# Performance work log

Hardware: AMD Instinct MI355X
Metric: run time of the kernel (lower is better)

## Reference

```python
import jax, jax.numpy as jnp
import numpy as np

N = 8192        # nodes
IN_DIM = 512    # input feature dim
H = 8           # heads (hardcoded as 8 in original forward)
HID = 64        # out_feats per head
T = 10          # top-K threshold from settings['T']
OUT = 3         # classes
NEG = -9e15
NE_HALF = 131072  # half edges; graph made symmetric -> 262144 edges


def setup_inputs() -> dict:
    key = jax.random.key(0)
    ks = jax.random.split(key, 10)
    feat = jax.random.normal(ks[0], (N, IN_DIM), jnp.float32)

    def edges(k):
        k1, k2, k3 = jax.random.split(k, 3)
        u = jax.random.randint(k1, (NE_HALF,), 0, N, jnp.int32)
        v = jax.random.randint(k2, (NE_HALF,), 0, N, jnp.int32)
        src = jnp.concatenate([u, v])
        dst = jnp.concatenate([v, u])
        t = jax.random.uniform(k3, (NE_HALF,), jnp.float32) * 0.1  # TransM values
        trans = jnp.concatenate([t, t])
        return src, dst, trans

    src0, dst0, trans0 = edges(ks[1])
    src1, dst1, trans1 = edges(ks[2])
    fc_w0 = jax.random.normal(ks[3], (IN_DIM, H * HID), jnp.float32) * 0.05
    fc_w1 = jax.random.normal(ks[4], (IN_DIM, H * HID), jnp.float32) * 0.05
    sem_w1 = jax.random.normal(ks[5], (H * HID, 128), jnp.float32) * 0.05
    sem_b1 = jnp.zeros((128,), jnp.float32)
    sem_w2 = jax.random.normal(ks[6], (128,), jnp.float32) * 0.05
    lin_w = jax.random.normal(ks[7], (H * HID, OUT), jnp.float32) * 0.05
    lin_b = jnp.zeros((OUT,), jnp.float32)
    return dict(feat=feat, src0=src0, dst0=dst0, trans0=trans0,
                src1=src1, dst1=dst1, trans1=trans1,
                fc_w0=fc_w0, fc_w1=fc_w1, sem_w1=sem_w1, sem_b1=sem_b1,
                sem_w2=sem_w2, lin_w=lin_w, lin_b=lin_b)


def _rohe_conv(feat, src, dst, trans, fc_w):
    f = (feat @ fc_w).reshape(N, H, HID)               # (N,H,HID) projected feats
    # per-edge per-head dot products (same math as dense matmul + edge gather)
    e = jnp.einsum('ehd,ehd->eh', f[src], f[dst])      # (Ne,H)
    vals = trans * e.sum(-1)                           # (Ne,)  (e * e_trans).sum over heads
    # dense sparse->to_dense attn matrix, duplicates coalesced by sum
    A = jnp.zeros((N, N), f.dtype).at[src, dst].add(vals)
    kth = jax.lax.top_k(A, T)[0][:, -1]                # per-row T-th largest
    thr = jnp.maximum(kth, 0.0)                        # clamp(min=0)
    Am = jnp.where(A < thr[:, None], NEG, A)
    gathered = Am[dst, src]                            # == Am.T[src, dst]
    e = jnp.where((gathered < -100.0)[:, None], NEG, e)
    # edge softmax grouped by destination node, per head
    m = jax.ops.segment_max(e, dst, num_segments=N)
    ex = jnp.exp(e - m[dst])
    s = jax.ops.segment_sum(ex, dst, num_segments=N)
    a = ex / s[dst]                                    # (Ne,H)
    # u_mul_e + sum aggregation
    out = jax.ops.segment_sum(f[src] * a[:, :, None], dst, num_segments=N)
    return jax.nn.elu(out).reshape(N, H * HID)         # activation=F.elu, flatten(1)


def reference(feat, src0, dst0, trans0, src1, dst1, trans1,
              fc_w0, fc_w1, sem_w1, sem_b1, sem_w2, lin_w, lin_b):
    z0 = _rohe_conv(feat, src0, dst0, trans0, fc_w0)
    z1 = _rohe_conv(feat, src1, dst1, trans1, fc_w1)
    z = jnp.stack([z0, z1], axis=1)                    # (N, M=2, D)
    # SemanticAttention: project -> tanh -> score, mean over nodes, softmax over metapaths
    w = jnp.tanh(z @ sem_w1 + sem_b1) @ sem_w2         # (N, M)
    beta = jax.nn.softmax(w.mean(0))                   # (M,)
    h = (z * beta[None, :, None]).sum(1)               # (N, D)
    return h @ lin_w + lin_b                           # final nn.Linear
```

## Files before the change

### kernel.cpp

```cpp
#include <hip/hip_runtime.h>
#include <math.h>

#define NN      8192
#define DIM     512
#define NHEAD   8
#define HID     64
#define NE      262144
#define NE_HALF 131072
#define CMASK   (NE_HALF - 1)
#define TOPK    10
#define NEGV    -9e15f
#define MAXD    160

typedef __attribute__((ext_vector_type(8))) short short8;
typedef __attribute__((ext_vector_type(4))) float f32x4;
typedef __attribute__((ext_vector_type(2))) int i32x2;
typedef __attribute__((ext_vector_type(4))) int i32x4;

__device__ __forceinline__ float bf2f(unsigned int h) {
    return __uint_as_float(h << 16);
}
__device__ __forceinline__ unsigned short f2bf(float x) {
    unsigned int u = __float_as_uint(x);
    unsigned int r = (u + 0x7fff + ((u >> 16) & 1)) >> 16;
    return (unsigned short)r;
}

__device__ __forceinline__ void scatter_body(int j, int c,
                                             const int* __restrict__ src0,
                                             const int* __restrict__ src1,
                                             const int* __restrict__ dst0,
                                             const int* __restrict__ dst1,
                                             const float* __restrict__ trans0,
                                             const float* __restrict__ trans1,
                                             int* curF, int* curC,
                                             i32x2* __restrict__ ed,
                                             i32x4* __restrict__ ce) {
    const int* s = c ? src1 : src0;
    const int* dt = c ? dst1 : dst0;
    int v = s[j];
    int dv = dt[j];
    int p = atomicAdd(&curF[c * NN + v], 1);
    i32x2 pk; pk.x = j; pk.y = dv;
    ed[c * NE + p] = pk;
    if (j < NE_HALF) {
        const float* tr = c ? trans1 : trans0;
        int q = atomicAdd(&curC[c * NN + v], 1);
        i32x4 ck;
        ck.x = j; ck.y = dv; ck.z = __float_as_int(tr[j]); ck.w = 0;
        ce[c * NE_HALF + q] = ck;
    }
}

__device__ __forceinline__ void split_w_body(const float* __restrict__ W,
                                             unsigned short* __restrict__ Th,
                                             unsigned short* __restrict__ Tl,
                                             int n0, int k0, int ncols,
                                             float (*t)[33], int tid) {
    int tx = tid & 31, ty = tid >> 5;
    #pragma unroll
    for (int i = 0; i < 4; i++)
        t[ty + 8 * i][tx] = W[(size_t)(k0 + ty + 8 * i) * ncols + n0 + tx];
    __syncthreads();
    #pragma unroll
    for (int i = 0; i < 4; i++) {
        float x = t[tx][ty + 8 * i];
        unsigned short h = f2bf(x);
        size_t off = (size_t)(n0 + ty + 8 * i) * DIM + k0 + tx;
        Th[off] = h;
        Tl[off] = f2bf(x - bf2f(h));
    }
}

__global__ __launch_bounds__(256) void prep(const float* __restrict__ feat,
                                            const float* __restrict__ w1,
                                            const float* __restrict__ fcw0,
                                            const float* __restrict__ fcw1,
                                            unsigned short* __restrict__ fH,
                                            unsigned short* __restrict__ fL,
                                            unsigned short* __restrict__ W1hT,
                                            unsigned short* __restrict__ W1lT,
                                            unsigned short* __restrict__ BhT0,
                                            unsigned short* __restrict__ BlT0,
                                            unsigned short* __restrict__ BhT1,
                                            unsigned short* __restrict__ BlT1,
                                            const int* __restrict__ src0,
                                            const int* __restrict__ src1,
                                            int* __restrict__ countsF,
                                            int* __restrict__ countsC) {
    int b = blockIdx.x;
    __shared__ float t[32][33];
    if (b < 4096) {
        int i = b * 256 + threadIdx.x;
        float4 v = ((const float4*)feat)[i];
        unsigned short h0 = f2bf(v.x), h1 = f2bf(v.y), h2 = f2bf(v.z), h3 = f2bf(v.w);
        ushort4 hv; hv.x = h0; hv.y = h1; hv.z = h2; hv.w = h3;
        ushort4 lv;
        lv.x = f2bf(v.x - bf2f(h0));
        lv.y = f2bf(v.y - bf2f(h1));
        lv.z = f2bf(v.z - bf2f(h2));
        lv.w = f2bf(v.w - bf2f(h3));
        ((ushort4*)fH)[i] = hv;
        ((ushort4*)fL)[i] = lv;
    } else if (b < 4160) {
        int idx = b - 4096;
        split_w_body(w1, W1hT, W1lT, (idx & 3) * 32, (idx >> 2) * 32, 128, t, threadIdx.x);
    } else if (b < 4416) {
        int idx = b - 4160;
        split_w_body(fcw0, BhT0, BlT0, (idx & 15) * 32, (idx >> 4) * 32, DIM, t, threadIdx.x);
    } else if (b < 4672) {
        int idx = b - 4416;
        split_w_body(fcw1, BhT1, BlT1, (idx & 15) * 32, (idx >> 4) * 32, DIM, t, threadIdx.x);
    } else {
        int sb = b - 4672;
        int c = sb >> 10;
        int j = (sb & 1023) * 256 + threadIdx.x;
        const int* s = c ? src1 : src0;
        int v = s[j];
        atomicAdd(&countsF[c * NN + v], 1);
        if (j < NE_HALF) atomicAdd(&countsC[c * NN + v], 1);
    }
}

__global__ __launch_bounds__(256) void gemm_mfma_sc(const unsigned short* __restrict__ Ah,
                                                    const unsigned short* __restrict__ Al,
                                                    const unsigned short* __restrict__ Bh,
                                                    const unsigned short* __restrict__ Bl,
                                                    float* __restrict__ Cf,
                                                    unsigned short* __restrict__ Ch,
                                                    const int* __restrict__ src0,
                                                    const int* __restrict__ src1,
                                                    const int* __restrict__ dst0,
                                                    const int* __restrict__ dst1,
                                                    const float* __restrict__ trans0,
                                                    const float* __restrict__ trans1,
                                                    int* curF, int* curC,
                                                    i32x2* __restrict__ ed,
                                                    i32x4* __restrict__ ce) {
    __shared__ unsigned short Ash[128][32];
    __shared__ unsigned short Asl[128][32];
    __shared__ unsigned short Bsh[64][32];
    __shared__ unsigned short Bsl[64][32];
    const int b = blockIdx.x;
    const int tid = threadIdx.x;
    if (b >= 512) {
        int sb = b - 512;
        int c = sb >> 10;
        int j = (sb & 1023) * 256 + tid;
        scatter_body(j, c, src0, src1, dst0, dst1, trans0, trans1,
                     curF, curC, ed, ce);
        return;
    }
    const int bm = (b >> 3) * 128;
    const int bn = (b & 7) * 64;
    const int lane = tid & 63;
    const int wave = tid >> 6;
    const int wm = (wave >> 1) * 64, wn = (wave & 1) * 32;
    const int fr = lane & 15, fq = lane >> 4;
    const int sr = tid >> 2, sc = (tid & 3) * 8;
    f32x4 acc[4][2] = {};
    const unsigned short* Ahg = Ah + (size_t)(bm + sr) * DIM + sc;
    const unsigned short* Alg = Al + (size_t)(bm + sr) * DIM + sc;
    const unsigned short* Bhg = Bh + (size_t)(bn + sr) * DIM + sc;
    const unsigned short* Blg = Bl + (size_t)(bn + sr) * DIM + sc;
    for (int kb = 0; kb < DIM; kb += 32) {
        __syncthreads();
        __builtin_amdgcn_global_load_lds(
            (const __attribute__((address_space(1))) void*)(Ahg + kb),
            (__attribute__((address_space(3))) void*)(&Ash[sr][sc]), 16, 0, 0);
        __builtin_amdgcn_global_load_lds(
            (const __attribute__((address_space(1))) void*)(Ahg + (size_t)64 * DIM + kb),
            (__attribute__((address_space(3))) void*)(&Ash[sr + 64][sc]), 16, 0, 0);
        __builtin_amdgcn_global_load_lds(
            (const __attribute__((address_space(1))) void*)(Alg + kb),
            (__attribute__((address_space(3))) void*)(&Asl[sr][sc]), 16, 0, 0);
        __builtin_amdgcn_global_load_lds(
            (const __attribute__((address_space(1))) void*)(Alg + (size_t)64 * DIM + kb),
            (__attribute__((address_space(3))) void*)(&Asl[sr + 64][sc]), 16, 0, 0);
        if (sr < 64) {
            __builtin_amdgcn_global_load_lds(
                (const __attribute__((address_space(1))) void*)(Bhg + kb),
                (__attribute__((address_space(3))) void*)(&Bsh[sr][sc]), 16, 0, 0);
            __builtin_amdgcn_global_load_lds(
                (const __attribute__((address_space(1))) void*)(Blg + kb),
                (__attribute__((address_space(3))) void*)(&Bsl[sr][sc]), 16, 0, 0);
        }
        __syncthreads();
        short8 ah[4], al[4], bh[2], bl[2];
        #pragma unroll
        for (int i = 0; i < 4; i++) {
            ah[i] = *(const short8*)&Ash[wm + i * 16 + fr][fq * 8];
            al[i] = *(const short8*)&Asl[wm + i * 16 + fr][fq * 8];
        }
        #pragma unroll
        for (int i = 0; i < 2; i++) {
            bh[i] = *(const short8*)&Bsh[wn + i * 16 + fr][fq * 8];
            bl[i] = *(const short8*)&Bsl[wn + i * 16 + fr][fq * 8];
        }
        #pragma unroll
        for (int mi = 0; mi < 4; mi++)
            #pragma unroll
            for (int ni = 0; ni < 2; ni++) {
                acc[mi][ni] = __builtin_amdgcn_mfma_f32_16x16x32_bf16(ah[mi], bh[ni], acc[mi][ni], 0, 0, 0);
                acc[mi][ni] = __builtin_amdgcn_mfma_f32_16x16x32_bf16(al[mi], bh[ni], acc[mi][ni], 0, 0, 0);
                acc[mi][ni] = __builtin_amdgcn_mfma_f32_16x16x32_bf16(ah[mi], bl[ni], acc[mi][ni], 0, 0, 0);
            }
    }
    #pragma unroll
    for (int mi = 0; mi < 4; mi++)
        #pragma unroll
        for (int ni = 0; ni < 2; ni++)
            #pragma unroll
            for (int r = 0; r < 4; r++) {
                int row = bm + wm + mi * 16 + fq * 4 + r;
                int col = bn + wn + ni * 16 + fr;
                float v = acc[mi][ni][r];
                size_t off = (size_t)row * DIM + col;
                Cf[off] = v;
                Ch[off] = f2bf(v);
            }
}

__global__ __launch_bounds__(256) void scan_offs4(const int* __restrict__ counts,
                                                  int* __restrict__ offs,
                                                  int* __restrict__ cur) {
    int b = blockIdx.x;
    counts += b * NN; offs += b * (NN + 1); cur += b * NN;
    __shared__ int part[256];
    int t = threadIdx.x;
    int base = t * 32;
    int s = 0;
    for (int i = 0; i < 32; i++) s += counts[base + i];
    part[t] = s;
    __syncthreads();
    if (t == 0) {
        int run = 0;
        for (int i = 0; i < 256; i++) { int v = part[i]; part[i] = run; run += v; }
        offs[NN] = run;
    }
    __syncthreads();
    int run = part[t];
    for (int i = 0; i < 32; i++) {
        offs[base + i] = run;
        cur[base + i] = run;
        run += counts[base + i];
    }
}

__global__ __launch_bounds__(256) void edge_dots_csr(const float* __restrict__ Cf,
                                                     const int* __restrict__ coffs,
                                                     const i32x4* __restrict__ ce,
                                                     float* __restrict__ e,
                                                     float* __restrict__ vals) {
    int n = blockIdx.x;
    int s0 = coffs[n];
    int d = coffs[n + 1] - s0;
    if (d <= 0) return;
    int wave = threadIdx.x >> 6, lane = threadIdx.x & 63;
    const float4* pf = (const float4*)(Cf + (size_t)n * DIM);
    float4 f0 = pf[lane * 2], f1 = pf[lane * 2 + 1];
    for (int i = wave; i < d; i += 8) {
        i32x4 c0e = ce[s0 + i];
        int j0 = c0e.x, dj0 = c0e.y;
        float t0 = __int_as_float(c0e.z);
        int i1 = i + 4;
        bool has1 = i1 < d;
        i32x4 c1e = has1 ? ce[s0 + i1] : c0e;
        int j1 = c1e.x, dj1 = c1e.y;
        float t1 = has1 ? __int_as_float(c1e.z) : 0.f;
        const float4* q0 = (const float4*)(Cf + (size_t)dj0 * DIM);
        const float4* q1 = (const float4*)(Cf + (size_t)dj1 * DIM);
        float4 b00 = q0[lane * 2], b01 = q0[lane * 2 + 1];
        float4 b10 = q1[lane * 2], b11 = q1[lane * 2 + 1];
        float p0, p1;
        p0  = f0.x * b00.x + f0.y * b00.y + f0.z * b00.z + f0.w * b00.w;
        p0 += f1.x * b01.x + f1.y * b01.y + f1.z * b01.z + f1.w * b01.w;
        p1  = f0.x * b10.x + f0.y * b10.y + f0.z * b10.z + f0.w * b10.w;
        p1 += f1.x * b11.x + f1.y * b11.y + f1.z * b11.z + f1.w * b11.w;
        p0 += __shfl_xor(p0, 1);
        p0 += __shfl_xor(p0, 2);
        p0 += __shfl_xor(p0, 4);
        p1 += __shfl_xor(p1, 1);
        p1 += __shfl_xor(p1, 2);
        p1 += __shfl_xor(p1, 4);
        if ((lane & 7) == 0) e[(size_t)j0 * NHEAD + (lane >> 3)] = p0;
        if (has1 && (lane & 7) == 0) e[(size_t)j1 * NHEAD + (lane >> 3)] = p1;
        p0 += __shfl_xor(p0, 8);
        p0 += __shfl_xor(p0, 16);
        p0 += __shfl_xor(p0, 32);
        p1 += __shfl_xor(p1, 8);
        p1 += __shfl_xor(p1, 16);
        p1 += __shfl_xor(p1, 32);
        if (lane == 0) {
            vals[j0] = t0 * p0;
            if (has1) vals[j1] = t1 * p1;
        }
    }
}

__global__ __launch_bounds__(256) void conv_post(const int* __restrict__ offs,
                                                 const i32x2* __restrict__ ed,
                                                 const float* __restrict__ e,
                                                 const float* __restrict__ vals,
                                                 const unsigned short* __restrict__ fb,
                                                 unsigned short* __restrict__ zb) {
    const int tid = threadIdx.x;
    const int w = tid >> 6, lane = tid & 63;
    const int n = blockIdx.x * 4 + w;
    int s0 = offs[n];
    int d = offs[n + 1] - s0;
    if (d > MAXD) d = MAXD;
    __shared__ int   ssrc[4][MAXD];
    __shared__ int   sjc[4][MAXD];
    __shared__ float sval[4][MAXD];
    __shared__ float svc[4][MAXD];
    __shared__ unsigned char lead[4][MAXD];
    __shared__ short sk[4][MAXD];
    __shared__ float sms[4][2][NHEAD];
    __shared__ int nkept[4];

    for (int i = lane; i < d; i += 64) {
        i32x2 pk = ed[s0 + i];
        int jc = pk.x & CMASK;
        sjc[w][i] = jc;
        ssrc[w][i] = pk.y;
        sval[w][i] = vals[jc];
    }
    __syncthreads();
    for (int i = lane; i < d; i += 64) {
        int c = ssrc[w][i];
        float sum = 0.f;
        bool leader = true;
        for (int k = 0; k < d; k++) {
            if (ssrc[w][k] == c) {
                sum += sval[w][k];
                if (k < i) leader = false;
            }
        }
        svc[w][i] = sum;
        lead[w][i] = leader ? 1 : 0;
    }
    __syncthreads();
    {
        float v[3];
        #pragma unroll
        for (int s = 0; s < 3; s++) v[s] = -1.f;
        int cnt = 0;
        #pragma unroll
        for (int s = 0; s < 3; s++) {
            int i = lane + s * 64;
            if (i < d && lead[w][i] && svc[w][i] > 0.f) { v[s] = svc[w][i]; cnt++; }
        }
        cnt += __shfl_xor(cnt, 1);  cnt += __shfl_xor(cnt, 2);
        cnt += __shfl_xor(cnt, 4);  cnt += __shfl_xor(cnt, 8);
        cnt += __shfl_xor(cnt, 16); cnt += __shfl_xor(cnt, 32);
        float thr = 0.f;
        if (cnt >= TOPK) {
            unsigned long long key = 0;
            for (int t = 0; t < TOPK; t++) {
                unsigned int bb = 0; int bs = 0;
                #pragma unroll
                for (int s = 0; s < 3; s++) {
                    if (v[s] > 0.f) {
                        unsigned int b = __float_as_uint(v[s]);
                        if (b > bb) { bb = b; bs = s; }
                    }
                }
                key = ((unsigned long long)bb << 12) | (unsigned)(lane << 3) | (unsigned)bs;
                unsigned long long o;
                o = __shfl_xor(key, 1);  if (o > key) key = o;
                o = __shfl_xor(key, 2);  if (o > key) key = o;
                o = __shfl_xor(key, 4);  if (o > key) key = o;
                o = __shfl_xor(key, 8);  if (o > key) key = o;
                o = __shfl_xor(key, 16); if (o > key) key = o;
                o = __shfl_xor(key, 32); if (o > key) key = o;
                int owner = (int)((key >> 3) & 63);
                if (owner == lane) v[key & 7] = -1.f;
            }
            thr = __uint_as_float((unsigned int)(key >> 12));
        }
        int base = 0;
        for (int s = 0; s * 64 < d; s++) {
            int i = s * 64 + lane;
            bool kp = (i < d) && (svc[w][i] >= thr);
            unsigned long long m = __ballot(kp);
            int pos = base + __popcll(m & ((1ull << lane) - 1ull));
            if (kp) sk[w][pos] = (short)i;
            base += (int)__popcll(m);
        }
        if (base == 0) {
            for (int i = lane; i < d; i += 64) sk[w][i] = (short)i;
            if (lane == 0) nkept[w] = -d;
        } else if (lane == 0) nkept[w] = base;
    }
    __syncthreads();
    int nk = nkept[w];
    bool uni = nk < 0;
    int dk = uni ? -nk : nk;
    if (!uni) {
        int h = lane & 7, sub = lane >> 3;
        float m = -INFINITY;
        for (int k = sub; k < dk; k += 8)
            m = fmaxf(m, e[(size_t)sjc[w][sk[w][k]] * NHEAD + h]);
        m = fmaxf(m, __shfl_xor(m, 8));
        m = fmaxf(m, __shfl_xor(m, 16));
        m = fmaxf(m, __shfl_xor(m, 32));
        float s = 0.f;
        for (int k = sub; k < dk; k += 8)
            s += expf(e[(size_t)sjc[w][sk[w][k]] * NHEAD + h] - m);
        s += __shfl_xor(s, 8);
        s += __shfl_xor(s, 16);
        s += __shfl_xor(s, 32);
        if (sub == 0) { sms[w][0][h] = m; sms[w][1][h] = s; }
    }
    __syncthreads();
    int c0 = lane * 8;
    int h = lane >> 3;
    float m = sms[w][0][h], s = sms[w][1][h];
    float invd = 1.0f / (float)d;
    float a0 = 0.f, a1 = 0.f, a2 = 0.f, a3 = 0.f;
    float a4 = 0.f, a5 = 0.f, a6 = 0.f, a7 = 0.f;
    for (int k = 0; k < dk; k++) {
        int ii = sk[w][k];
        float wgt = uni ? invd
                        : expf(e[(size_t)sjc[w][ii] * NHEAD + h] - m) / s;
        uint4 v = *(const uint4*)(fb + (size_t)ssrc[w][ii] * DIM + c0);
        a0 += wgt * bf2f(v.x & 0xffffu); a1 += wgt * bf2f(v.x >> 16);
        a2 += wgt * bf2f(v.y & 0xffffu); a3 += wgt * bf2f(v.y >> 16);
        a4 += wgt * bf2f(v.z & 0xffffu); a5 += wgt * bf2f(v.z >> 16);
        a6 += wgt * bf2f(v.w & 0xffffu); a7 += wgt * bf2f(v.w >> 16);
    }
    a0 = a0 > 0.f ? a0 : expf(a0) - 1.f;
    a1 = a1 > 0.f ? a1 : expf(a1) - 1.f;
    a2 = a2 > 0.f ? a2 : expf(a2) - 1.f;
    a3 = a3 > 0.f ? a3 : expf(a3) - 1.f;
    a4 = a4 > 0.f ? a4 : expf(a4) - 1.f;
    a5 = a5 > 0.f ? a5 : expf(a5) - 1.f;
    a6 = a6 > 0.f ? a6 : expf(a6) - 1.f;
    a7 = a7 > 0.f ? a7 : expf(a7) - 1.f;
    uint4 o;
    o.x = (unsigned)f2bf(a0) | ((unsigned)f2bf(a1) << 16);
    o.y = (unsigned)f2bf(a2) | ((unsigned)f2bf(a3) << 16);
    o.z = (unsigned)f2bf(a4) | ((unsigned)f2bf(a5) << 16);
    o.w = (unsigned)f2bf(a6) | ((unsigned)f2bf(a7) << 16);
    *(uint4*)(zb + (size_t)n * DIM + c0) = o;
}

__global__ __launch_bounds__(256) void sem_scores3(const unsigned short* __restrict__ z0,
                                                   const unsigned short* __restrict__ z1,
                                                   const unsigned short* __restrict__ W1hT,
                                                   const unsigned short* __restrict__ W1lT,
                                                   const float* __restrict__ b1,
                                                   const float* __restrict__ w2,
                                                   float* wsum) {
    const unsigned short* Z = blockIdx.y ? z1 : z0;
    const int bm = blockIdx.x * 64;
    const int tid = threadIdx.x;
    const int lane = tid & 63, wave = tid >> 6;
    const int fr = lane & 15, fq = lane >> 4;
    __shared__ unsigned short Zs[64][32];
    __shared__ unsigned short Wh[128][32];
    __shared__ unsigned short Wl[128][32];
    const int sr = tid >> 2, sc = (tid & 3) * 8;
    f32x4 acc[8] = {};
    const unsigned short* Zg  = Z    + (size_t)(bm + sr) * DIM + sc;
    const unsigned short* Whg = W1hT + (size_t)sr * DIM + sc;
    const unsigned short* Wlg = W1lT + (size_t)sr * DIM + sc;
    for (int kb = 0; kb < DIM; kb += 32) {
        __syncthreads();
        __builtin_amdgcn_global_load_lds(
            (const __attribute__((address_space(1))) void*)(Zg + kb),
            (__attribute__((address_space(3))) void*)(&Zs[sr][sc]), 16, 0, 0);
        __builtin_amdgcn_global_load_lds(
            (const __attribute__((address_space(1))) void*)(Whg + kb),
            (__attribute__((address_space(3))) void*)(&Wh[sr][sc]), 16, 0, 0);
        __builtin_amdgcn_global_load_lds(
            (const __attribute__((address_space(1))) void*)(Whg + (size_t)64 * DIM + kb),
            (__attribute__((address_space(3))) void*)(&Wh[sr + 64][sc]), 16, 0, 0);
        __builtin_amdgcn_global_load_lds(
            (const __attribute__((address_space(1))) void*)(Wlg + kb),
            (__attribute__((address_space(3))) void*)(&Wl[sr][sc]), 16, 0, 0);
        __builtin_amdgcn_global_load_lds(
            (const __attribute__((address_space(1))) void*)(Wlg + (size_t)64 * DIM + kb),
            (__attribute__((address_space(3))) void*)(&Wl[sr + 64][sc]), 16, 0, 0);
        __syncthreads();
        short8 af = *(const short8*)&Zs[wave * 16 + fr][fq * 8];
        #pragma unroll
        for (int ni = 0; ni < 8; ni++) {
            short8 bh = *(const short8*)&Wh[ni * 16 + fr][fq * 8];
            acc[ni] = __builtin_amdgcn_mfma_f32_16x16x32_bf16(af, bh, acc[ni], 0, 0, 0);
        }
        #pragma unroll
        for (int ni = 0; ni < 8; ni++) {
            short8 bl = *(const short8*)&Wl[ni * 16 + fr][fq * 8];
            acc[ni] = __builtin_amdgcn_mfma_f32_16x16x32_bf16(af, bl, acc[ni], 0, 0, 0);
        }
    }
    float local = 0.f;
    #pragma unroll
    for (int ni = 0; ni < 8; ni++) {
        int col = ni * 16 + fr;
        float bb = b1[col], ww = w2[col];
        #pragma unroll
        for (int r = 0; r < 4; r++)
            local += tanhf(acc[ni][r] + bb) * ww;
    }
    __shared__ float red[256];
    red[tid] = local;
    __syncthreads();
    for (int s = 128; s > 0; s >>= 1) {
        if (tid < s) red[tid] += red[tid + s];
        __syncthreads();
    }
    if (tid == 0) atomicAdd(&wsum[blockIdx.y], red[0]);
}

__global__ __launch_bounds__(256) void final_out(const unsigned short* __restrict__ z0,
                                                 const unsigned short* __restrict__ z1,
                                                 const float* __restrict__ wsum,
                                                 const float* __restrict__ lin_w,
                                                 const float* __restrict__ lin_b,
                                                 float* __restrict__ out) {
    int idx = blockIdx.x * 256 + threadIdx.x;
    int n = idx / 3, o = idx - n * 3;
    float w0 = wsum[0] * (1.0f / NN), w1v = wsum[1] * (1.0f / NN);
    float mx = fmaxf(w0, w1v);
    float e0 = expf(w0 - mx), e1 = expf(w1v - mx);
    float beta0 = e0 / (e0 + e1), beta1 = e1 / (e0 + e1);
    const unsigned short* p0 = z0 + (size_t)n * DIM;
    const unsigned short* p1 = z1 + (size_t)n * DIM;
    float acc = 0.f;
    for (int dd = 0; dd < DIM; dd++)
        acc += (beta0 * bf2f(p0[dd]) + beta1 * bf2f(p1[dd])) * lin_w[dd * 3 + o];
    out[idx] = acc + lin_b[o];
}

extern "C" void kernel_launch(void* const* d_in, const int* in_sizes, int n_in,
                              void* d_out, int out_size, void* d_ws, size_t ws_size,
                              hipStream_t stream) {
    const float* feat = (const float*)d_in[0];
    const int*   srcp[2]   = { (const int*)d_in[1], (const int*)d_in[4] };
    const int*   dstp[2]   = { (const int*)d_in[2], (const int*)d_in[5] };
    const float* transp[2] = { (const float*)d_in[3], (const float*)d_in[6] };
    const float* fcw[2]    = { (const float*)d_in[7], (const float*)d_in[8] };
    const float* sem_w1 = (const float*)d_in[9];
    const float* sem_b1 = (const float*)d_in[10];
    const float* sem_w2 = (const float*)d_in[11];
    const float* lin_w  = (const float*)d_in[12];
    const float* lin_b  = (const float*)d_in[13];
    float* out = (float*)d_out;

    char* ws = (char*)d_ws;
    const size_t MB = 1 << 20;
    const size_t KB = 1 << 10;
    if (ws_size < 76 * MB) return;
    float*          Cf    = (float*)(ws);
    unsigned short* Ch    = (unsigned short*)(ws + 16 * MB);
    unsigned short* z0    = (unsigned short*)(ws + 24 * MB);
    unsigned short* z1    = (unsigned short*)(ws + 32 * MB);
    unsigned short* fH    = (unsigned short*)(ws + 40 * MB);
    unsigned short* fL    = (unsigned short*)(ws + 48 * MB);
    float*          e     = (float*)(ws + 56 * MB);
    float*          vals  = (float*)(ws + 60 * MB);
    i32x2*          ed    = (i32x2*)(ws + 60 * MB + 512 * KB);
    i32x4*          ce    = (i32x4*)(ws + 64 * MB + 512 * KB);
    unsigned short* BhT0  = (unsigned short*)(ws + 68 * MB + 512 * KB);
    unsigned short* BlT0  = (unsigned short*)(ws + 69 * MB);
    unsigned short* BhT1  = (unsigned short*)(ws + 69 * MB + 512 * KB);
    unsigned short* BlT1  = (unsigned short*)(ws + 70 * MB);
    unsigned short* W1hT  = (unsigned short*)(ws + 70 * MB + 512 * KB);
    unsigned short* W1lT  = (unsigned short*)(ws + 70 * MB + 640 * KB);
    int*            counts= (int*)  (ws + 70 * MB + 768 * KB);
    int*            offs  = (int*)  (ws + 70 * MB + 896 * KB);
    int*            cur   = (int*)  (ws + 71 * MB + 128 * KB);
    float*          wsum  = (float*)(ws + 71 * MB + 256 * KB);

    hipMemsetAsync(counts, 0, 4 * NN * sizeof(int), stream);
    prep<<<6720, 256, 0, stream>>>(feat, sem_w1, fcw[0], fcw[1],
                                   fH, fL, W1hT, W1lT, BhT0, BlT0, BhT1, BlT1,
                                   srcp[0], srcp[1], counts, counts + 2 * NN);
    scan_offs4<<<4, 256, 0, stream>>>(counts, offs, cur);
    for (int c = 0; c < 2; c++) {
        unsigned short* z = c ? z1 : z0;
        const int* offsF = offs + c * (NN + 1);
        const int* offsC = offs + (2 + c) * (NN + 1);
        const unsigned short* Bh = c ? BhT1 : BhT0;
        const unsigned short* Bl = c ? BlT1 : BlT0;
        int nblk = (c == 0) ? 2560 : 512;
        gemm_mfma_sc<<<nblk, 256, 0, stream>>>(fH, fL, Bh, Bl, Cf, Ch,
                                               srcp[0], srcp[1], dstp[0], dstp[1],
                                               transp[0], transp[1],
                                               cur, cur + 2 * NN, ed, ce);
        edge_dots_csr<<<NN, 256, 0, stream>>>(Cf, offsC, ce + c * NE_HALF, e, vals);
        conv_post<<<NN / 4, 256, 0, stream>>>(offsF, ed + c * NE, e, vals, Ch, z);
    }
    hipMemsetAsync(wsum, 0, 2 * sizeof(float), stream);
    sem_scores3<<<dim3(NN / 64, 2), 256, 0, stream>>>(z0, z1, W1hT, W1lT, sem_b1, sem_w2, wsum);
    final_out<<<(NN * 3) / 256, 256, 0, stream>>>(z0, z1, wsum, lin_w, lin_b, out);
}
```

Measured before the change: 386.1 us.

## Fuse metapath stages across kernels with double-buffered intermediates to overlap work

Splits the per-metapath intermediate buffers (projected features, edge scores, vals) into separate copies for each metapath so the stages of the two metapaths can run in the same launches. The GEMM for metapath 1 now shares a launch with metapath 0's edge dots, and metapath 0's conv shares a launch with metapath 1's edge dots, so there are fewer sequential launches and less tail idle time. The cost is a larger workspace and heterogeneous blocks within a launch, with possible LDS-driven occupancy limits when the GEMM and edge bodies share a kernel.

```diff
diff --git a/kernel.cpp b/kernel.cpp
--- a/kernel.cpp
+++ b/kernel.cpp
@@ -50,6 +50,288 @@
         ck.x = j; ck.y = dv; ck.z = __float_as_int(tr[j]); ck.w = 0;
         ce[c * NE_HALF + q] = ck;
     }
+}
+
+__device__ __forceinline__ void gemm_body(int b,
+                                          const unsigned short* __restrict__ Ah,
+                                          const unsigned short* __restrict__ Al,
+                                          const unsigned short* __restrict__ Bh,
+                                          const unsigned short* __restrict__ Bl,
+                                          float* __restrict__ Cf,
+                                          unsigned short* __restrict__ Ch) {
+    __shared__ unsigned short Ash[128][32];
+    __shared__ unsigned short Asl[128][32];
+    __shared__ unsigned short Bsh[64][32];
+    __shared__ unsigned short Bsl[64][32];
+    const int bm = (b >> 3) * 128;
+    const int bn = (b & 7) * 64;
+    const int tid = threadIdx.x;
+    const int lane = tid & 63;
+    const int wave = tid >> 6;
+    const int wm = (wave >> 1) * 64, wn = (wave & 1) * 32;
+    const int fr = lane & 15, fq = lane >> 4;
+    const int sr = tid >> 2, sc = (tid & 3) * 8;
+    f32x4 acc[4][2] = {};
+    const unsigned short* Ahg = Ah + (size_t)(bm + sr) * DIM + sc;
+    const unsigned short* Alg = Al + (size_t)(bm + sr) * DIM + sc;
+    const unsigned short* Bhg = Bh + (size_t)(bn + sr) * DIM + sc;
+    const unsigned short* Blg = Bl + (size_t)(bn + sr) * DIM + sc;
+    for (int kb = 0; kb < DIM; kb += 32) {
+        __syncthreads();
+        __builtin_amdgcn_global_load_lds(
+            (const __attribute__((address_space(1))) void*)(Ahg + kb),
+            (__attribute__((address_space(3))) void*)(&Ash[sr][sc]), 16, 0, 0);
+        __builtin_amdgcn_global_load_lds(
+            (const __attribute__((address_space(1))) void*)(Ahg + (size_t)64 * DIM + kb),
+            (__attribute__((address_space(3))) void*)(&Ash[sr + 64][sc]), 16, 0, 0);
+        __builtin_amdgcn_global_load_lds(
+            (const __attribute__((address_space(1))) void*)(Alg + kb),
+            (__attribute__((address_space(3))) void*)(&Asl[sr][sc]), 16, 0, 0);
+        __builtin_amdgcn_global_load_lds(
+            (const __attribute__((address_space(1))) void*)(Alg + (size_t)64 * DIM + kb),
+            (__attribute__((address_space(3))) void*)(&Asl[sr + 64][sc]), 16, 0, 0);
+        if (sr < 64) {
+            __builtin_amdgcn_global_load_lds(
+                (const __attribute__((address_space(1))) void*)(Bhg + kb),
+                (__attribute__((address_space(3))) void*)(&Bsh[sr][sc]), 16, 0, 0);
+            __builtin_amdgcn_global_load_lds(
+                (const __attribute__((address_space(1))) void*)(Blg + kb),
+                (__attribute__((address_space(3))) void*)(&Bsl[sr][sc]), 16, 0, 0);
+        }
+        __syncthreads();
+        short8 ah[4], al[4], bh[2], bl[2];
+        #pragma unroll
+        for (int i = 0; i < 4; i++) {
+            ah[i] = *(const short8*)&Ash[wm + i * 16 + fr][fq * 8];
+            al[i] = *(const short8*)&Asl[wm + i * 16 + fr][fq * 8];
+        }
+        #pragma unroll
+        for (int i = 0; i < 2; i++) {
+            bh[i] = *(const short8*)&Bsh[wn + i * 16 + fr][fq * 8];
+            bl[i] = *(const short8*)&Bsl[wn + i * 16 + fr][fq * 8];
+        }
+        #pragma unroll
+        for (int mi = 0; mi < 4; mi++)
+            #pragma unroll
+            for (int ni = 0; ni < 2; ni++) {
+                acc[mi][ni] = __builtin_amdgcn_mfma_f32_16x16x32_bf16(ah[mi], bh[ni], acc[mi][ni], 0, 0, 0);
+                acc[mi][ni] = __builtin_amdgcn_mfma_f32_16x16x32_bf16(al[mi], bh[ni], acc[mi][ni], 0, 0, 0);
+                acc[mi][ni] = __builtin_amdgcn_mfma_f32_16x16x32_bf16(ah[mi], bl[ni], acc[mi][ni], 0, 0, 0);
+            }
+    }
+    #pragma unroll
+    for (int mi = 0; mi < 4; mi++)
+        #pragma unroll
+        for (int ni = 0; ni < 2; ni++)
+            #pragma unroll
+            for (int r = 0; r < 4; r++) {
+                int row = bm + wm + mi * 16 + fq * 4 + r;
+                int col = bn + wn + ni * 16 + fr;
+                float v = acc[mi][ni][r];
+                size_t off = (size_t)row * DIM + col;
+                Cf[off] = v;
+                Ch[off] = f2bf(v);
+            }
+}
+
+__device__ __forceinline__ void edge_body(int n,
+                                          const float* __restrict__ Cf,
+                                          const int* __restrict__ coffs,
+                                          const i32x4* __restrict__ ce,
+                                          float* __restrict__ e,
+                                          float* __restrict__ vals) {
+    int s0 = coffs[n];
+    int d = coffs[n + 1] - s0;
+    if (d <= 0) return;
+    int wave = threadIdx.x >> 6, lane = threadIdx.x & 63;
+    const float4* pf = (const float4*)(Cf + (size_t)n * DIM);
+    float4 f0 = pf[lane * 2], f1 = pf[lane * 2 + 1];
+    for (int i = wave; i < d; i += 8) {
+        i32x4 c0e = ce[s0 + i];
+        int j0 = c0e.x, dj0 = c0e.y;
+        float t0 = __int_as_float(c0e.z);
+        int i1 = i + 4;
+        bool has1 = i1 < d;
+        i32x4 c1e = has1 ? ce[s0 + i1] : c0e;
+        int j1 = c1e.x, dj1 = c1e.y;
+        float t1 = has1 ? __int_as_float(c1e.z) : 0.f;
+        const float4* q0 = (const float4*)(Cf + (size_t)dj0 * DIM);
+        const float4* q1 = (const float4*)(Cf + (size_t)dj1 * DIM);
+        float4 b00 = q0[lane * 2], b01 = q0[lane * 2 + 1];
+        float4 b10 = q1[lane * 2], b11 = q1[lane * 2 + 1];
+        float p0, p1;
+        p0  = f0.x * b00.x + f0.y * b00.y + f0.z * b00.z + f0.w * b00.w;
+        p0 += f1.x * b01.x + f1.y * b01.y + f1.z * b01.z + f1.w * b01.w;
+        p1  = f0.x * b10.x + f0.y * b10.y + f0.z * b10.z + f0.w * b10.w;
+        p1 += f1.x * b11.x + f1.y * b11.y + f1.z * b11.z + f1.w * b11.w;
+        p0 += __shfl_xor(p0, 1);
+        p0 += __shfl_xor(p0, 2);
+        p0 += __shfl_xor(p0, 4);
+        p1 += __shfl_xor(p1, 1);
+        p1 += __shfl_xor(p1, 2);
+        p1 += __shfl_xor(p1, 4);
+        if ((lane & 7) == 0) e[(size_t)j0 * NHEAD + (lane >> 3)] = p0;
+        if (has1 && (lane & 7) == 0) e[(size_t)j1 * NHEAD + (lane >> 3)] = p1;
+        p0 += __shfl_xor(p0, 8);
+        p0 += __shfl_xor(p0, 16);
+        p0 += __shfl_xor(p0, 32);
+        p1 += __shfl_xor(p1, 8);
+        p1 += __shfl_xor(p1, 16);
+        p1 += __shfl_xor(p1, 32);
+        if (lane == 0) {
+            vals[j0] = t0 * p0;
+            if (has1) vals[j1] = t1 * p1;
+        }
+    }
+}
+
+__device__ __forceinline__ void conv_body(int blk,
+                                          const int* __restrict__ offs,
+                                          const i32x2* __restrict__ ed,
+                                          const float* __restrict__ e,
+                                          const float* __restrict__ vals,
+                                          const unsigned short* __restrict__ fb,
+                                          unsigned short* __restrict__ zb) {
+    const int tid = threadIdx.x;
+    const int w = tid >> 6, lane = tid & 63;
+    const int n = blk * 4 + w;
+    int s0 = offs[n];
+    int d = offs[n + 1] - s0;
+    if (d > MAXD) d = MAXD;
+    __shared__ int   ssrc[4][MAXD];
+    __shared__ int   sjc[4][MAXD];
+    __shared__ float sval[4][MAXD];
+    __shared__ float svc[4][MAXD];
+    __shared__ unsigned char lead[4][MAXD];
+    __shared__ short sk[4][MAXD];
+    __shared__ float sms[4][2][NHEAD];
+    __shared__ int nkept[4];
+
+    for (int i = lane; i < d; i += 64) {
+        i32x2 pk = ed[s0 + i];
+        int jc = pk.x & CMASK;
+        sjc[w][i] = jc;
+        ssrc[w][i] = pk.y;
+        sval[w][i] = vals[jc];
+    }
+    __syncthreads();
+    for (int i = lane; i < d; i += 64) {
+        int c = ssrc[w][i];
+        float sum = 0.f;
+        bool leader = true;
+        for (int k = 0; k < d; k++) {
+            if (ssrc[w][k] == c) {
+                sum += sval[w][k];
+                if (k < i) leader = false;
+            }
+        }
+        svc[w][i] = sum;
+        lead[w][i] = leader ? 1 : 0;
+    }
+    __syncthreads();
+    {
+        float v[3];
+        #pragma unroll
+        for (int s = 0; s < 3; s++) v[s] = -1.f;
+        int cnt = 0;
+        #pragma unroll
+        for (int s = 0; s < 3; s++) {
+            int i = lane + s * 64;
+            if (i < d && lead[w][i] && svc[w][i] > 0.f) { v[s] = svc[w][i]; cnt++; }
+        }
+        cnt += __shfl_xor(cnt, 1);  cnt += __shfl_xor(cnt, 2);
+        cnt += __shfl_xor(cnt, 4);  cnt += __shfl_xor(cnt, 8);
+        cnt += __shfl_xor(cnt, 16); cnt += __shfl_xor(cnt, 32);
+        float thr = 0.f;
+        if (cnt >= TOPK) {
+            unsigned long long key = 0;
+            for (int t = 0; t < TOPK; t++) {
+                unsigned int bb = 0; int bs = 0;
+                #pragma unroll
+                for (int s = 0; s < 3; s++) {
+                    if (v[s] > 0.f) {
+                        unsigned int b = __float_as_uint(v[s]);
+                        if (b > bb) { bb = b; bs = s; }
+                    }
+                }
+                key = ((unsigned long long)bb << 12) | (unsigned)(lane << 3) | (unsigned)bs;
+                unsigned long long o;
+                o = __shfl_xor(key, 1);  if (o > key) key = o;
+                o = __shfl_xor(key, 2);  if (o > key) key = o;
+                o = __shfl_xor(key, 4);  if (o > key) key = o;
+                o = __shfl_xor(key, 8);  if (o > key) key = o;
+                o = __shfl_xor(key, 16); if (o > key) key = o;
+                o = __shfl_xor(key, 32); if (o > key) key = o;
+                int owner = (int)((key >> 3) & 63);
+                if (owner == lane) v[key & 7] = -1.f;
+            }
+            thr = __uint_as_float((unsigned int)(key >> 12));
+        }
+        int base = 0;
+        for (int s = 0; s * 64 < d; s++) {
+            int i = s * 64 + lane;
+            bool kp = (i < d) && (svc[w][i] >= thr);
+            unsigned long long m = __ballot(kp);
+            int pos = base + __popcll(m & ((1ull << lane) - 1ull));
+            if (kp) sk[w][pos] = (short)i;
+            base += (int)__popcll(m);
+        }
+        if (base == 0) {
+            for (int i = lane; i < d; i += 64) sk[w][i] = (short)i;
+            if (lane == 0) nkept[w] = -d;
+        } else if (lane == 0) nkept[w] = base;
+    }
+    __syncthreads();
+    int nk = nkept[w];
+    bool uni = nk < 0;
+    int dk = uni ? -nk : nk;
+    if (!uni) {
+        int h = lane & 7, sub = lane >> 3;
+        float m = -INFINITY;
+        for (int k = sub; k < dk; k += 8)
+            m = fmaxf(m, e[(size_t)sjc[w][sk[w][k]] * NHEAD + h]);
+        m = fmaxf(m, __shfl_xor(m, 8));
+        m = fmaxf(m, __shfl_xor(m, 16));
+        m = fmaxf(m, __shfl_xor(m, 32));
+        float s = 0.f;
+        for (int k = sub; k < dk; k += 8)
+            s += expf(e[(size_t)sjc[w][sk[w][k]] * NHEAD + h] - m);
+        s += __shfl_xor(s, 8);
+        s += __shfl_xor(s, 16);
+        s += __shfl_xor(s, 32);
+        if (sub == 0) { sms[w][0][h] = m; sms[w][1][h] = s; }
+    }
+    __syncthreads();
+    int c0 = lane * 8;
+    int h = lane >> 3;
+    float m = sms[w][0][h], s = sms[w][1][h];
+    float invd = 1.0f / (float)d;
+    float a0 = 0.f, a1 = 0.f, a2 = 0.f, a3 = 0.f;
+    float a4 = 0.f, a5 = 0.f, a6 = 0.f, a7 = 0.f;
+    for (int k = 0; k < dk; k++) {
+        int ii = sk[w][k];
+        float wgt = uni ? invd
+                        : expf(e[(size_t)sjc[w][ii] * NHEAD + h] - m) / s;
+        uint4 v = *(const uint4*)(fb + (size_t)ssrc[w][ii] * DIM + c0);
+        a0 += wgt * bf2f(v.x & 0xffffu); a1 += wgt * bf2f(v.x >> 16);
+        a2 += wgt * bf2f(v.y & 0xffffu); a3 += wgt * bf2f(v.y >> 16);
+        a4 += wgt * bf2f(v.z & 0xffffu); a5 += wgt * bf2f(v.z >> 16);
+        a6 += wgt * bf2f(v.w & 0xffffu); a7 += wgt * bf2f(v.w >> 16);
+    }
+    a0 = a0 > 0.f ? a0 : expf(a0) - 1.f;
+    a1 = a1 > 0.f ? a1 : expf(a1) - 1.f;
+    a2 = a2 > 0.f ? a2 : expf(a2) - 1.f;
+    a3 = a3 > 0.f ? a3 : expf(a3) - 1.f;
+    a4 = a4 > 0.f ? a4 : expf(a4) - 1.f;
+    a5 = a5 > 0.f ? a5 : expf(a5) - 1.f;
+    a6 = a6 > 0.f ? a6 : expf(a6) - 1.f;
+    a7 = a7 > 0.f ? a7 : expf(a7) - 1.f;
+    uint4 o;
+    o.x = (unsigned)f2bf(a0) | ((unsigned)f2bf(a1) << 16);
+    o.y = (unsigned)f2bf(a2) | ((unsigned)f2bf(a3) << 16);
+    o.z = (unsigned)f2bf(a4) | ((unsigned)f2bf(a5) << 16);
+    o.w = (unsigned)f2bf(a6) | ((unsigned)f2bf(a7) << 16);
+    *(uint4*)(zb + (size_t)n * DIM + c0) = o;
 }
 
 __device__ __forceinline__ void split_w_body(const float* __restrict__ W,
@@ -122,105 +404,6 @@
     }
 }
 
-__global__ __launch_bounds__(256) void gemm_mfma_sc(const unsigned short* __restrict__ Ah,
-                                                    const unsigned short* __restrict__ Al,
-                                                    const unsigned short* __restrict__ Bh,
-                                                    const unsigned short* __restrict__ Bl,
-                                                    float* __restrict__ Cf,
-                                                    unsigned short* __restrict__ Ch,
-                                                    const int* __restrict__ src0,
-                                                    const int* __restrict__ src1,
-                                                    const int* __restrict__ dst0,
-                                                    const int* __restrict__ dst1,
-                                                    const float* __restrict__ trans0,
-                                                    const float* __restrict__ trans1,
-                                                    int* curF, int* curC,
-                                                    i32x2* __restrict__ ed,
-                                                    i32x4* __restrict__ ce) {
-    __shared__ unsigned short Ash[128][32];
-    __shared__ unsigned short Asl[128][32];
-    __shared__ unsigned short Bsh[64][32];
-    __shared__ unsigned short Bsl[64][32];
-    const int b = blockIdx.x;
-    const int tid = threadIdx.x;
-    if (b >= 512) {
-        int sb = b - 512;
-        int c = sb >> 10;
-        int j = (sb & 1023) * 256 + tid;
-        scatter_body(j, c, src0, src1, dst0, dst1, trans0, trans1,
-                     curF, curC, ed, ce);
-        return;
-    }
-    const int bm = (b >> 3) * 128;
-    const int bn = (b & 7) * 64;
-    const int lane = tid & 63;
-    const int wave = tid >> 6;
-    const int wm = (wave >> 1) * 64, wn = (wave & 1) * 32;
-    const int fr = lane & 15, fq = lane >> 4;
-    const int sr = tid >> 2, sc = (tid & 3) * 8;
-    f32x4 acc[4][2] = {};
-    const unsigned short* Ahg = Ah + (size_t)(bm + sr) * DIM + sc;
-    const unsigned short* Alg = Al + (size_t)(bm + sr) * DIM + sc;
-    const unsigned short* Bhg = Bh + (size_t)(bn + sr) * DIM + sc;
-    const unsigned short* Blg = Bl + (size_t)(bn + sr) * DIM + sc;
-    for (int kb = 0; kb < DIM; kb += 32) {
-        __syncthreads();
-        __builtin_amdgcn_global_load_lds(
-            (const __attribute__((address_space(1))) void*)(Ahg + kb),
-            (__attribute__((address_space(3))) void*)(&Ash[sr][sc]), 16, 0, 0);
-        __builtin_amdgcn_global_load_lds(
-            (const __attribute__((address_space(1))) void*)(Ahg + (size_t)64 * DIM + kb),
-            (__attribute__((address_space(3))) void*)(&Ash[sr + 64][sc]), 16, 0, 0);
-        __builtin_amdgcn_global_load_lds(
-            (const __attribute__((address_space(1))) void*)(Alg + kb),
-            (__attribute__((address_space(3))) void*)(&Asl[sr][sc]), 16, 0, 0);
-        __builtin_amdgcn_global_load_lds(
-            (const __attribute__((address_space(1))) void*)(Alg + (size_t)64 * DIM + kb),
-            (__attribute__((address_space(3))) void*)(&Asl[sr + 64][sc]), 16, 0, 0);
-        if (sr < 64) {
-            __builtin_amdgcn_global_load_lds(
-                (const __attribute__((address_space(1))) void*)(Bhg + kb),
-                (__attribute__((address_space(3))) void*)(&Bsh[sr][sc]), 16, 0, 0);
-            __builtin_amdgcn_global_load_lds(
-                (const __attribute__((address_space(1))) void*)(Blg + kb),
-                (__attribute__((address_space(3))) void*)(&Bsl[sr][sc]), 16, 0, 0);
-        }
-        __syncthreads();
-        short8 ah[4], al[4], bh[2], bl[2];
-        #pragma unroll
-        for (int i = 0; i < 4; i++) {
-            ah[i] = *(const short8*)&Ash[wm + i * 16 + fr][fq * 8];
-            al[i] = *(const short8*)&Asl[wm + i * 16 + fr][fq * 8];
-        }
-        #pragma unroll
-        for (int i = 0; i < 2; i++) {
-            bh[i] = *(const short8*)&Bsh[wn + i * 16 + fr][fq * 8];
-            bl[i] = *(const short8*)&Bsl[wn + i * 16 + fr][fq * 8];
-        }
-        #pragma unroll
-        for (int mi = 0; mi < 4; mi++)
-            #pragma unroll
-            for (int ni = 0; ni < 2; ni++) {
-                acc[mi][ni] = __builtin_amdgcn_mfma_f32_16x16x32_bf16(ah[mi], bh[ni], acc[mi][ni], 0, 0, 0);
-                acc[mi][ni] = __builtin_amdgcn_mfma_f32_16x16x32_bf16(al[mi], bh[ni], acc[mi][ni], 0, 0, 0);
-                acc[mi][ni] = __builtin_amdgcn_mfma_f32_16x16x32_bf16(ah[mi], bl[ni], acc[mi][ni], 0, 0, 0);
-            }
-    }
-    #pragma unroll
-    for (int mi = 0; mi < 4; mi++)
-        #pragma unroll
-        for (int ni = 0; ni < 2; ni++)
-            #pragma unroll
-            for (int r = 0; r < 4; r++) {
-                int row = bm + wm + mi * 16 + fq * 4 + r;
-                int col = bn + wn + ni * 16 + fr;
-                float v = acc[mi][ni][r];
-                size_t off = (size_t)row * DIM + col;
-                Cf[off] = v;
-                Ch[off] = f2bf(v);
-            }
-}
-
 __global__ __launch_bounds__(256) void scan_offs4(const int* __restrict__ counts,
                                                   int* __restrict__ offs,
                                                   int* __restrict__ cur) {
@@ -247,54 +430,68 @@
     }
 }
 
-__global__ __launch_bounds__(256) void edge_dots_csr(const float* __restrict__ Cf,
-                                                     const int* __restrict__ coffs,
-                                                     const i32x4* __restrict__ ce,
-                                                     float* __restrict__ e,
-                                                     float* __restrict__ vals) {
-    int n = blockIdx.x;
-    int s0 = coffs[n];
-    int d = coffs[n + 1] - s0;
-    if (d <= 0) return;
-    int wave = threadIdx.x >> 6, lane = threadIdx.x & 63;
-    const float4* pf = (const float4*)(Cf + (size_t)n * DIM);
-    float4 f0 = pf[lane * 2], f1 = pf[lane * 2 + 1];
-    for (int i = wave; i < d; i += 8) {
-        i32x4 c0e = ce[s0 + i];
-        int j0 = c0e.x, dj0 = c0e.y;
-        float t0 = __int_as_float(c0e.z);
-        int i1 = i + 4;
-        bool has1 = i1 < d;
-        i32x4 c1e = has1 ? ce[s0 + i1] : c0e;
-        int j1 = c1e.x, dj1 = c1e.y;
-        float t1 = has1 ? __int_as_float(c1e.z) : 0.f;
-        const float4* q0 = (const float4*)(Cf + (size_t)dj0 * DIM);
-        const float4* q1 = (const float4*)(Cf + (size_t)dj1 * DIM);
-        float4 b00 = q0[lane * 2], b01 = q0[lane * 2 + 1];
-        float4 b10 = q1[lane * 2], b11 = q1[lane * 2 + 1];
-        float p0, p1;
-        p0  = f0.x * b00.x + f0.y * b00.y + f0.z * b00.z + f0.w * b00.w;
-        p0 += f1.x * b01.x + f1.y * b01.y + f1.z * b01.z + f1.w * b01.w;
-        p1  = f0.x * b10.x + f0.y * b10.y + f0.z * b10.z + f0.w * b10.w;
-        p1 += f1.x * b11.x + f1.y * b11.y + f1.z * b11.z + f1.w * b11.w;
-        p0 += __shfl_xor(p0, 1);
-        p0 += __shfl_xor(p0, 2);
-        p0 += __shfl_xor(p0, 4);
-        p1 += __shfl_xor(p1, 1);
-        p1 += __shfl_xor(p1, 2);
-        p1 += __shfl_xor(p1, 4);
-        if ((lane & 7) == 0) e[(size_t)j0 * NHEAD + (lane >> 3)] = p0;
-        if (has1 && (lane & 7) == 0) e[(size_t)j1 * NHEAD + (lane >> 3)] = p1;
-        p0 += __shfl_xor(p0, 8);
-        p0 += __shfl_xor(p0, 16);
-        p0 += __shfl_xor(p0, 32);
-        p1 += __shfl_xor(p1, 8);
-        p1 += __shfl_xor(p1, 16);
-        p1 += __shfl_xor(p1, 32);
-        if (lane == 0) {
-            vals[j0] = t0 * p0;
-            if (has1) vals[j1] = t1 * p1;
-        }
+__global__ __launch_bounds__(256) void gemm_sc(const unsigned short* __restrict__ Ah,
+                                               const unsigned short* __restrict__ Al,
+                                               const unsigned short* __restrict__ Bh,
+                                               const unsigned short* __restrict__ Bl,
+                                               float* __restrict__ Cf,
+                                               unsigned short* __restrict__ Ch,
+                                               const int* __restrict__ src0,
+                                               const int* __restrict__ src1,
+                                               const int* __restrict__ dst0,
+                                               const int* __restrict__ dst1,
+                                               const float* __restrict__ trans0,
+                                               const float* __restrict__ trans1,
+                                               int* curF, int* curC,
+                                               i32x2* __restrict__ ed,
+                                               i32x4* __restrict__ ce) {
+    int b = blockIdx.x;
+    if (b < 512) {
+        gemm_body(b, Ah, Al, Bh, Bl, Cf, Ch);
+    } else {
+        int sb = b - 512;
+        int c = sb >> 10;
+        int j = (sb & 1023) * 256 + threadIdx.x;
+        scatter_body(j, c, src0, src1, dst0, dst1, trans0, trans1,
+                     curF, curC, ed, ce);
+    }
+}
+
+__global__ __launch_bounds__(256) void gemm_ed(const unsigned short* __restrict__ Ah,
+                                               const unsigned short* __restrict__ Al,
+                                               const unsigned short* __restrict__ Bh,
+                                               const unsigned short* __restrict__ Bl,
+                                               float* __restrict__ Cf1,
+                                               unsigned short* __restrict__ Ch1,
+                                               const float* __restrict__ Cf0,
+                                               const int* __restrict__ coffs0,
+                                               const i32x4* __restrict__ ce0,
+                                               float* __restrict__ e0,
+                                               float* __restrict__ vals0) {
+    int b = blockIdx.x;
+    if (b < 512) {
+        gemm_body(b, Ah, Al, Bh, Bl, Cf1, Ch1);
+    } else {
+        edge_body(b - 512, Cf0, coffs0, ce0, e0, vals0);
+    }
+}
+
+__global__ __launch_bounds__(256) void conv_ed(const int* __restrict__ offsF0,
+                                               const i32x2* __restrict__ ed0,
+                                               const float* __restrict__ e0,
+                                               const float* __restrict__ vals0,
+                                               const unsigned short* __restrict__ Ch0,
+                                               unsigned short* __restrict__ z0,
+                                               const float* __restrict__ Cf1,
+                                               const int* __restrict__ coffs1,
+                                               const i32x4* __restrict__ ce1,
+                                               float* __restrict__ e1,
+                                               float* __restrict__ vals1) {
+    int b = blockIdx.x;
+    if (b < 2048) {
+        conv_body(b, offsF0, ed0, e0, vals0, Ch0, z0);
+    } else {
+        edge_body(b - 2048, Cf1, coffs1, ce1, e1, vals1);
     }
 }
 
@@ -304,146 +501,7 @@
                                                  const float* __restrict__ vals,
                                                  const unsigned short* __restrict__ fb,
                                                  unsigned short* __restrict__ zb) {
-    const int tid = threadIdx.x;
-    const int w = tid >> 6, lane = tid & 63;
-    const int n = blockIdx.x * 4 + w;
-    int s0 = offs[n];
-    int d = offs[n + 1] - s0;
-    if (d > MAXD) d = MAXD;
-    __shared__ int   ssrc[4][MAXD];
-    __shared__ int   sjc[4][MAXD];
-    __shared__ float sval[4][MAXD];
-    __shared__ float svc[4][MAXD];
-    __shared__ unsigned char lead[4][MAXD];
-    __shared__ short sk[4][MAXD];
-    __shared__ float sms[4][2][NHEAD];
-    __shared__ int nkept[4];
-
-    for (int i = lane; i < d; i += 64) {
-        i32x2 pk = ed[s0 + i];
-        int jc = pk.x & CMASK;
-        sjc[w][i] = jc;
-        ssrc[w][i] = pk.y;
-        sval[w][i] = vals[jc];
-    }
-    __syncthreads();
-    for (int i = lane; i < d; i += 64) {
-        int c = ssrc[w][i];
-        float sum = 0.f;
-        bool leader = true;
-        for (int k = 0; k < d; k++) {
-            if (ssrc[w][k] == c) {
-                sum += sval[w][k];
-                if (k < i) leader = false;
-            }
-        }
-        svc[w][i] = sum;
-        lead[w][i] = leader ? 1 : 0;
-    }
-    __syncthreads();
-    {
-        float v[3];
-        #pragma unroll
-        for (int s = 0; s < 3; s++) v[s] = -1.f;
-        int cnt = 0;
-        #pragma unroll
-        for (int s = 0; s < 3; s++) {
-            int i = lane + s * 64;
-            if (i < d && lead[w][i] && svc[w][i] > 0.f) { v[s] = svc[w][i]; cnt++; }
-        }
-        cnt += __shfl_xor(cnt, 1);  cnt += __shfl_xor(cnt, 2);
-        cnt += __shfl_xor(cnt, 4);  cnt += __shfl_xor(cnt, 8);
-        cnt += __shfl_xor(cnt, 16); cnt += __shfl_xor(cnt, 32);
-        float thr = 0.f;
-        if (cnt >= TOPK) {
-            unsigned long long key = 0;
-            for (int t = 0; t < TOPK; t++) {
-                unsigned int bb = 0; int bs = 0;
-                #pragma unroll
-                for (int s = 0; s < 3; s++) {
-                    if (v[s] > 0.f) {
-                        unsigned int b = __float_as_uint(v[s]);
-                        if (b > bb) { bb = b; bs = s; }
-                    }
-                }
-                key = ((unsigned long long)bb << 12) | (unsigned)(lane << 3) | (unsigned)bs;
-                unsigned long long o;
-                o = __shfl_xor(key, 1);  if (o > key) key = o;
-                o = __shfl_xor(key, 2);  if (o > key) key = o;
-                o = __shfl_xor(key, 4);  if (o > key) key = o;
-                o = __shfl_xor(key, 8);  if (o > key) key = o;
-                o = __shfl_xor(key, 16); if (o > key) key = o;
-                o = __shfl_xor(key, 32); if (o > key) key = o;
-                int owner = (int)((key >> 3) & 63);
-                if (owner == lane) v[key & 7] = -1.f;
-            }
-            thr = __uint_as_float((unsigned int)(key >> 12));
-        }
-        int base = 0;
-        for (int s = 0; s * 64 < d; s++) {
-            int i = s * 64 + lane;
-            bool kp = (i < d) && (svc[w][i] >= thr);
-            unsigned long long m = __ballot(kp);
-            int pos = base + __popcll(m & ((1ull << lane) - 1ull));
-            if (kp) sk[w][pos] = (short)i;
-            base += (int)__popcll(m);
-        }
-        if (base == 0) {
-            for (int i = lane; i < d; i += 64) sk[w][i] = (short)i;
-            if (lane == 0) nkept[w] = -d;
-        } else if (lane == 0) nkept[w] = base;
-    }
-    __syncthreads();
-    int nk = nkept[w];
-    bool uni = nk < 0;
-    int dk = uni ? -nk : nk;
-    if (!uni) {
-        int h = lane & 7, sub = lane >> 3;
-        float m = -INFINITY;
-        for (int k = sub; k < dk; k += 8)
-            m = fmaxf(m, e[(size_t)sjc[w][sk[w][k]] * NHEAD + h]);
-        m = fmaxf(m, __shfl_xor(m, 8));
-        m = fmaxf(m, __shfl_xor(m, 16));
-        m = fmaxf(m, __shfl_xor(m, 32));
-        float s = 0.f;
-        for (int k = sub; k < dk; k += 8)
-            s += expf(e[(size_t)sjc[w][sk[w][k]] * NHEAD + h] - m);
-        s += __shfl_xor(s, 8);
-        s += __shfl_xor(s, 16);
-        s += __shfl_xor(s, 32);
-        if (sub == 0) { sms[w][0][h] = m; sms[w][1][h] = s; }
-    }
-    __syncthreads();
-    int c0 = lane * 8;
-    int h = lane >> 3;
-    float m = sms[w][0][h], s = sms[w][1][h];
-    float invd = 1.0f / (float)d;
-    float a0 = 0.f, a1 = 0.f, a2 = 0.f, a3 = 0.f;
-    float a4 = 0.f, a5 = 0.f, a6 = 0.f, a7 = 0.f;
-    for (int k = 0; k < dk; k++) {
-        int ii = sk[w][k];
-        float wgt = uni ? invd
-                        : expf(e[(size_t)sjc[w][ii] * NHEAD + h] - m) / s;
-        uint4 v = *(const uint4*)(fb + (size_t)ssrc[w][ii] * DIM + c0);
-        a0 += wgt * bf2f(v.x & 0xffffu); a1 += wgt * bf2f(v.x >> 16);
-        a2 += wgt * bf2f(v.y & 0xffffu); a3 += wgt * bf2f(v.y >> 16);
-        a4 += wgt * bf2f(v.z & 0xffffu); a5 += wgt * bf2f(v.z >> 16);
-        a6 += wgt * bf2f(v.w & 0xffffu); a7 += wgt * bf2f(v.w >> 16);
-    }
-    a0 = a0 > 0.f ? a0 : expf(a0) - 1.f;
-    a1 = a1 > 0.f ? a1 : expf(a1) - 1.f;
-    a2 = a2 > 0.f ? a2 : expf(a2) - 1.f;
-    a3 = a3 > 0.f ? a3 : expf(a3) - 1.f;
-    a4 = a4 > 0.f ? a4 : expf(a4) - 1.f;
-    a5 = a5 > 0.f ? a5 : expf(a5) - 1.f;
-    a6 = a6 > 0.f ? a6 : expf(a6) - 1.f;
-    a7 = a7 > 0.f ? a7 : expf(a7) - 1.f;
-    uint4 o;
-    o.x = (unsigned)f2bf(a0) | ((unsigned)f2bf(a1) << 16);
-    o.y = (unsigned)f2bf(a2) | ((unsigned)f2bf(a3) << 16);
-    o.z = (unsigned)f2bf(a4) | ((unsigned)f2bf(a5) << 16);
-    o.w = (unsigned)f2bf(a6) | ((unsigned)f2bf(a7) << 16);
-    *(uint4*)(zb + (size_t)n * DIM + c0) = o;
+    conv_body(blockIdx.x, offs, ed, e, vals, fb, zb);
 }
 
 __global__ __launch_bounds__(256) void sem_scores3(const unsigned short* __restrict__ z0,
@@ -553,47 +611,50 @@
     char* ws = (char*)d_ws;
     const size_t MB = 1 << 20;
     const size_t KB = 1 << 10;
-    if (ws_size < 76 * MB) return;
-    float*          Cf    = (float*)(ws);
-    unsigned short* Ch    = (unsigned short*)(ws + 16 * MB);
-    unsigned short* z0    = (unsigned short*)(ws + 24 * MB);
-    unsigned short* z1    = (unsigned short*)(ws + 32 * MB);
-    unsigned short* fH    = (unsigned short*)(ws + 40 * MB);
-    unsigned short* fL    = (unsigned short*)(ws + 48 * MB);
-    float*          e     = (float*)(ws + 56 * MB);
-    float*          vals  = (float*)(ws + 60 * MB);
-    i32x2*          ed    = (i32x2*)(ws + 60 * MB + 512 * KB);
-    i32x4*          ce    = (i32x4*)(ws + 64 * MB + 512 * KB);
-    unsigned short* BhT0  = (unsigned short*)(ws + 68 * MB + 512 * KB);
-    unsigned short* BlT0  = (unsigned short*)(ws + 69 * MB);
-    unsigned short* BhT1  = (unsigned short*)(ws + 69 * MB + 512 * KB);
-    unsigned short* BlT1  = (unsigned short*)(ws + 70 * MB);
-    unsigned short* W1hT  = (unsigned short*)(ws + 70 * MB + 512 * KB);
-    unsigned short* W1lT  = (unsigned short*)(ws + 70 * MB + 640 * KB);
-    int*            counts= (int*)  (ws + 70 * MB + 768 * KB);
-    int*            offs  = (int*)  (ws + 70 * MB + 896 * KB);
-    int*            cur   = (int*)  (ws + 71 * MB + 128 * KB);
-    float*          wsum  = (float*)(ws + 71 * MB + 256 * KB);
+    if (ws_size < 101 * MB) return;
+    float*          Cf0   = (float*)(ws);
+    float*          Cf1   = (float*)(ws + 16 * MB);
+    unsigned short* Ch0   = (unsigned short*)(ws + 32 * MB);
+    unsigned short* Ch1   = (unsigned short*)(ws + 40 * MB);
+    unsigned short* z0    = (unsigned short*)(ws + 48 * MB);
+    unsigned short* z1    = (unsigned short*)(ws + 56 * MB);
+    unsigned short* fH    = (unsigned short*)(ws + 64 * MB);
+    unsigned short* fL    = (unsigned short*)(ws + 72 * MB);
+    float*          e0    = (float*)(ws + 80 * MB);
+    float*          e1    = (float*)(ws + 84 * MB);
+    float*          vals0 = (float*)(ws + 88 * MB);
+    float*          vals1 = (float*)(ws + 88 * MB + 512 * KB);
+    i32x2*          ed    = (i32x2*)(ws + 89 * MB);
+    i32x4*          ce    = (i32x4*)(ws + 93 * MB);
+    unsigned short* BhT0  = (unsigned short*)(ws + 97 * MB);
+    unsigned short* BlT0  = (unsigned short*)(ws + 97 * MB + 512 * KB);
+    unsigned short* BhT1  = (unsigned short*)(ws + 98 * MB);
+    unsigned short* BlT1  = (unsigned short*)(ws + 98 * MB + 512 * KB);
+    unsigned short* W1hT  = (unsigned short*)(ws + 99 * MB);
+    unsigned short* W1lT  = (unsigned short*)(ws + 99 * MB + 128 * KB);
+    int*            counts= (int*)  (ws + 99 * MB + 256 * KB);
+    int*            offs  = (int*)  (ws + 99 * MB + 384 * KB);
+    int*            cur   = (int*)  (ws + 99 * MB + 576 * KB);
+    float*          wsum  = (float*)(ws + 99 * MB + 704 * KB);
 
     hipMemsetAsync(counts, 0, 4 * NN * sizeof(int), stream);
     prep<<<6720, 256, 0, stream>>>(feat, sem_w1, fcw[0], fcw[1],
                                    fH, fL, W1hT, W1lT, BhT0, BlT0, BhT1, BlT1,
                                    srcp[0], srcp[1], counts, counts + 2 * NN);
     scan_offs4<<<4, 256, 0, stream>>>(counts, offs, cur);
-    for (int c = 0; c < 2; c++) {
-        unsigned short* z = c ? z1 : z0;
-        const int* offsF = offs + c * (NN + 1);
-        const int* offsC = offs + (2 + c) * (NN + 1);
-        const unsigned short* Bh = c ? BhT1 : BhT0;
-        const unsigned short* Bl = c ? BlT1 : BlT0;
-        int nblk = (c == 0) ? 2560 : 512;
-        gemm_mfma_sc<<<nblk, 256, 0, stream>>>(fH, fL, Bh, Bl, Cf, Ch,
-                                               srcp[0], srcp[1], dstp[0], dstp[1],
-                                               transp[0], transp[1],
-                                               cur, cur + 2 * NN, ed, ce);
-        edge_dots_csr<<<NN, 256, 0, stream>>>(Cf, offsC, ce + c * NE_HALF, e, vals);
-        conv_post<<<NN / 4, 256, 0, stream>>>(offsF, ed + c * NE, e, vals, Ch, z);
-    }
+    const int* offsF0 = offs;
+    const int* offsF1 = offs + (NN + 1);
+    const int* offsC0 = offs + 2 * (NN + 1);
+    const int* offsC1 = offs + 3 * (NN + 1);
+    gemm_sc<<<2560, 256, 0, stream>>>(fH, fL, BhT0, BlT0, Cf0, Ch0,
+                                      srcp[0], srcp[1], dstp[0], dstp[1],
+                                      transp[0], transp[1],
+                                      cur, cur + 2 * NN, ed, ce);
+    gemm_ed<<<8704, 256, 0, stream>>>(fH, fL, BhT1, BlT1, Cf1, Ch1,
+                                      Cf0, offsC0, ce, e0, vals0);
+    conv_ed<<<10240, 256, 0, stream>>>(offsF0, ed, e0, vals0, Ch0, z0,
+                                       Cf1, offsC1, ce + NE_HALF, e1, vals1);
+    conv_post<<<2048, 256, 0, stream>>>(offsF1, ed + NE, e1, vals1, Ch1, z1);
     hipMemsetAsync(wsum, 0, 2 * sizeof(float), stream);
     sem_scores3<<<dim3(NN / 64, 2), 256, 0, stream>>>(z0, z1, W1hT, W1lT, sem_b1, sem_w2, wsum);
     final_out<<<(NN * 3) / 256, 256, 0, stream>>>(z0, z1, wsum, lin_w, lin_b, out);
```

Measured after the change: 377.8 us. -2.2%, faster.
